# Optimization experiments

Measured on AMD Instinct MI355X. Metric: run time of the kernel, lower is better.

Reference implementation:

```python
import jax, jax.numpy as jnp
import numpy as np

N_ANGLES = 8
K = 15


def setup_inputs() -> dict:
    key = jax.random.key(0)
    k1, k2, k3 = jax.random.split(key, 3)
    N, Cin, Cout = 2048, 16, 32
    NA = N_ANGLES * N
    x = jax.random.normal(k1, (N, Cin), dtype=jnp.float32)
    # scaled so spectral radius ~1 (like a normalized Laplacian) to keep the
    # Chebyshev recurrence numerically bounded
    Ls = jax.random.normal(k2, (NA, NA), dtype=jnp.float32) / np.float32(np.sqrt(NA))
    fan = N_ANGLES * Cin + Cout  # xavier_uniform bound
    bound = np.float32(np.sqrt(6.0 / fan))
    weight = jax.random.uniform(k3, (K, N_ANGLES * Cin, Cout), dtype=jnp.float32,
                                minval=-bound, maxval=bound)
    bias = jnp.zeros((Cout,), dtype=jnp.float32)
    return {"x": x, "Ls": Ls, "weight": weight, "bias": bias}


def _proj(T, Wk, N, Cin):
    # T: [n_angles*N, Cin] -> [N, n_angles*Cin] @ Wk -> [N, Cout]
    return T.reshape(N_ANGLES, N, Cin).transpose(1, 0, 2).reshape(N, N_ANGLES * Cin) @ Wk


def reference(x, Ls, weight, bias):
    N, Cin = x.shape
    Tx0 = jnp.tile(x, (N_ANGLES, 1))            # [nA*N, Cin]
    out = _proj(Tx0, weight[0], N, Cin)          # [N, Cout]
    Tx1 = Ls @ Tx0
    out = out + _proj(Tx1, weight[1], N, Cin)
    for k in range(2, K):
        Tx2 = 2.0 * (Ls @ Tx1) - Tx0
        out = out + _proj(Tx2, weight[k], N, Cin)
        Tx0, Tx1 = Tx1, Tx2
    return out + bias
```

## Files before the change

kernel.cpp:

```cpp
#include <hip/hip_runtime.h>
#include <hip/hip_fp16.h>

#define NA   16384
#define NN   2048
#define CIN  16
#define COUT 32
#define NANG 8
#define KCH  15
#define NSTEP  512
#define CHUNK  4
#define NCHUNK (NSTEP / CHUNK)
#define NPANEL 1024
#define PGRID  ((NN * COUT) / 256)
#define SGRID  (NPANEL / 4)

#define TSCALE_INV 0.03125f
#define TSCALE     32.0f


typedef _Float16 f16x8 __attribute__((ext_vector_type(8)));
typedef _Float16 f16x4 __attribute__((ext_vector_type(4)));
typedef float    f32x4 __attribute__((ext_vector_type(4)));

__global__ __launch_bounds__(256) void k_tile_t(const float* __restrict__ x,
                                                float* __restrict__ T32,
                                                _Float16* __restrict__ Tsw) {
    int tid = blockIdx.x * 256 + threadIdx.x;
    if (tid >= 8 * 64 * 64) return;
    const int s  = tid >> 12;
    const int st = (tid >> 6) & 63;
    const int l  = tid & 63;
    const int ch = l & 15;
    const int c2 = ((l >> 4) << 3) + (st << 5);
    f16x8 h;
    float v[8];
    #pragma unroll
    for (int e = 0; e < 8; ++e) {
        v[e] = x[(c2 + e) * CIN + ch];
        h[e] = (_Float16)(v[e] * TSCALE_INV);
    }
    float* d = T32 + (size_t)ch * NA + s * (NA / 8) + c2;
    *(float4*)(d)     = make_float4(v[0], v[1], v[2], v[3]);
    *(float4*)(d + 4) = make_float4(v[4], v[5], v[6], v[7]);
    *(f16x8*)(Tsw + (size_t)tid * 8) = h;
}

__device__ __forceinline__ void proj_body(const float* __restrict__ Tt,
                                          const float* __restrict__ W,
                                          const float* __restrict__ bias,
                                          float* __restrict__ out, int add,
                                          int idx) {
    const int n  = idx >> 5;
    const int co = idx & 31;
    float s = add ? out[idx] : bias[co];
    #pragma unroll
    for (int a = 0; a < NANG; ++a)
        #pragma unroll
        for (int ci = 0; ci < CIN; ++ci)
            s = fmaf(Tt[(size_t)ci * NA + a * NN + n],
                     W[(size_t)(a * CIN + ci) * COUT + co], s);
    out[idx] = s;
}

#define LOADCHUNK(BUF, PC)                                                   \
    _Pragma("unroll")                                                        \
    for (int u = 0; u < CHUNK; ++u) {                                        \
        const int st = (PC) * CHUNK + u;                                     \
        if (CONV) {                                                          \
            f32x4 f0 = __builtin_nontemporal_load((const f32x4*)(aF + (size_t)st * 32));     \
            f32x4 f1 = __builtin_nontemporal_load((const f32x4*)(aF + (size_t)st * 32 + 4)); \
            f16x8 h;                                                         \
            h[0] = (_Float16)f0[0]; h[1] = (_Float16)f0[1];                  \
            h[2] = (_Float16)f0[2]; h[3] = (_Float16)f0[3];                  \
            h[4] = (_Float16)f1[0]; h[5] = (_Float16)f1[1];                  \
            h[6] = (_Float16)f1[2]; h[7] = (_Float16)f1[3];                  \
            __builtin_nontemporal_store(h, (f16x8*)(aW + (size_t)st * 512)); \
            A[BUF][u] = h;                                                   \
        } else {                                                             \
            A[BUF][u] = __builtin_nontemporal_load((const f16x8*)(aP + (size_t)st * 512));   \
        }                                                                    \
        B[BUF][u] = *(const f16x8*)(bP + (size_t)st * 512);                  \
    }

template<int CONV, int REV>
__global__ __launch_bounds__(256)
void k_sweep(const float* __restrict__ Ls,
             _Float16* __restrict__ Lsw,
             const _Float16* __restrict__ Tsw,
             const float* __restrict__ Tp,
             float* __restrict__ Tn,
             _Float16* __restrict__ Tswn,
             float alpha, float beta,
             const float* __restrict__ Tproj,
             const float* __restrict__ Wk,
             const float* __restrict__ bias,
             float* __restrict__ out, int add) {
    if (blockIdx.x < PGRID) {
        proj_body(Tproj, Wk, bias, out, add,
                  (int)blockIdx.x * 256 + (int)threadIdx.x);
        return;
    }
    constexpr int DEPTH = CONV ? 2 : 4;
    static_assert(NCHUNK % 2 == 0 && NCHUNK % 4 == 0,
                  "tail chunk would replay stale buffer");
    const int w    = threadIdx.x >> 6;
    const int l    = threadIdx.x & 63;
    const int bid0 = (int)blockIdx.x - PGRID;
    const int bid  = REV ? (SGRID - 1 - bid0) : bid0;
    const int p    = bid * 4 + w;
    const int rc   = l & 15;
    const int kg   = l >> 4;

    const size_t aoff = (size_t)p * (NSTEP * 512) + (size_t)l * 8;
    const _Float16* aP = Lsw + aoff;
    _Float16*       aW = Lsw + aoff;
    const float*    aF = Ls + (size_t)(p * 16 + rc) * NA + kg * 8;
    const _Float16* bP = Tsw + (size_t)l * 8;

    f32x4 acc = {0.f, 0.f, 0.f, 0.f};
    f16x8 A[DEPTH][CHUNK], B[DEPTH][CHUNK];

    LOADCHUNK(0, 0);
    if (DEPTH >= 3) { LOADCHUNK(1 & (DEPTH - 1), 1); }
    if (DEPTH >= 4) { LOADCHUNK(2 & (DEPTH - 1), 2); }

    #pragma unroll 1
    for (int cc = 0; cc < NCHUNK; cc += DEPTH) {
        #pragma unroll
        for (int d = 0; d < DEPTH; ++d) {
            const int pf = cc + d + DEPTH - 1;
            if (pf < NCHUNK) { LOADCHUNK((d + DEPTH - 1) % DEPTH, pf); }
            #pragma unroll
            for (int u = 0; u < CHUNK; ++u)
                acc = __builtin_amdgcn_mfma_f32_16x16x32_f16(A[d][u], B[d][u],
                                                             acc, 0, 0, 0);
        }
    }

    const size_t tb = (size_t)rc * NA + (size_t)p * 16 + kg * 4;
    float4 tp4 = make_float4(0.f, 0.f, 0.f, 0.f);
    if (beta != 0.f) tp4 = *(const float4*)(Tp + tb);
    const float v0 = alpha * acc[0] + beta * tp4.x;
    const float v1 = alpha * acc[1] + beta * tp4.y;
    const float v2 = alpha * acc[2] + beta * tp4.z;
    const float v3 = alpha * acc[3] + beta * tp4.w;
    *(float4*)(Tn + tb) = make_float4(v0, v1, v2, v3);
    const int c0 = p * 16 + kg * 4;
    const size_t tf = ((size_t)(c0 >> 5) * 64 + ((c0 >> 3) & 3) * 16 + rc) * 8
                      + (c0 & 7);
    f16x4 h;
    h[0] = (_Float16)(v0 * TSCALE_INV); h[1] = (_Float16)(v1 * TSCALE_INV);
    h[2] = (_Float16)(v2 * TSCALE_INV); h[3] = (_Float16)(v3 * TSCALE_INV);
    *(f16x4*)(Tswn + tf) = h;
}

__global__ __launch_bounds__(256) void k_proj_t(const float* __restrict__ Tt,
                                                const float* __restrict__ W,
                                                const float* __restrict__ bias,
                                                float* __restrict__ out, int add) {
    int idx = blockIdx.x * 256 + threadIdx.x;
    if (idx >= NN * COUT) return;
    proj_body(Tt, W, bias, out, add, idx);
}

extern "C" void kernel_launch(void* const* d_in, const int* in_sizes, int n_in,
                              void* d_out, int out_size, void* d_ws, size_t ws_size,
                              hipStream_t stream) {
    const float* x    = (const float*)d_in[0];
    const float* Ls   = (const float*)d_in[1];
    const float* W    = (const float*)d_in[2];
    const float* bias = (const float*)d_in[3];
    float* out = (float*)d_out;

    char* wsb = (char*)d_ws;
    _Float16* Lsw = (_Float16*)wsb;
    float* T32base = (float*)(wsb + (size_t)NA * NA * sizeof(_Float16));
    const size_t TSZ = (size_t)CIN * NA;
    float* T32[3] = { T32base, T32base + TSZ, T32base + 2 * TSZ };
    _Float16* Tswbase = (_Float16*)(T32base + 3 * TSZ);
    _Float16* Tsw[3] = { Tswbase, Tswbase + TSZ, Tswbase + 2 * TSZ };

    const int WSTRIDE = (NANG * CIN) * COUT;
    const int FGRID = (8 * 64 * 64) / 256;
    const int GRID  = PGRID + SGRID;

    k_tile_t<<<FGRID, 256, 0, stream>>>(x, T32[0], Tsw[0]);

    k_sweep<1, 0><<<GRID, 256, 0, stream>>>(Ls, Lsw, Tsw[0], T32[0],
                                            T32[1], Tsw[1], TSCALE, 0.f,
                                            T32[0], W, bias, out, 0);

    int prev = 0, cur = 1;
    for (int k = 2; k < KCH; ++k) {
        int nxt = 3 - cur - prev;
        const float* Wk = W + (size_t)(k - 1) * WSTRIDE;
        if (k & 1)
            k_sweep<0, 0><<<GRID, 256, 0, stream>>>(Ls, Lsw, Tsw[cur], T32[prev],
                                                    T32[nxt], Tsw[nxt],
                                                    2.0f * TSCALE, -1.f,
                                                    T32[cur], Wk, bias, out, 1);
        else
            k_sweep<0, 1><<<GRID, 256, 0, stream>>>(Ls, Lsw, Tsw[cur], T32[prev],
                                                    T32[nxt], Tsw[nxt],
                                                    2.0f * TSCALE, -1.f,
                                                    T32[cur], Wk, bias, out, 1);
        prev = cur; cur = nxt;
    }

    k_proj_t<<<PGRID, 256, 0, stream>>>(T32[cur], W + (size_t)(KCH - 1) * WSTRIDE,
                                        bias, out, 1);
}
```

Measured before the change: 1.686 ms.

## Fuse all Chebyshev steps into one cooperative persistent kernel with grid syncs

Replaces the sequence of per-step kernel launches with a single cooperative kernel of 256 blocks. It runs the tile, projection and sweep stages in a loop separated by grid-wide barriers, and projection work is spread over all blocks before each sweep. The Ls fp16 copy is written with normal rather than nontemporal stores in the fused path, so it may stay in cache. The intent is to remove launch gaps and keep data warm, but only 256 blocks run, which may leave CUs underused. The multi-launch path is kept as a fallback.

Result: slower. 2.408 ms (+42.8%).

```diff
diff --git a/kernel.cpp b/kernel.cpp
--- a/kernel.cpp
+++ b/kernel.cpp
@@ -1,5 +1,8 @@
 #include <hip/hip_runtime.h>
 #include <hip/hip_fp16.h>
+#include <hip/hip_cooperative_groups.h>
+
+namespace cg = cooperative_groups;
 
 #define NA   16384
 #define NN   2048
@@ -13,6 +16,8 @@
 #define NPANEL 1024
 #define PGRID  ((NN * COUT) / 256)
 #define SGRID  (NPANEL / 4)
+#define TGRID  ((8 * 64 * 64) / 256)
+#define WSTRIDE (NANG * CIN * COUT)
 
 #define TSCALE_INV 0.03125f
 #define TSCALE     32.0f
@@ -22,11 +27,10 @@
 typedef _Float16 f16x4 __attribute__((ext_vector_type(4)));
 typedef float    f32x4 __attribute__((ext_vector_type(4)));
 
-__global__ __launch_bounds__(256) void k_tile_t(const float* __restrict__ x,
-                                                float* __restrict__ T32,
-                                                _Float16* __restrict__ Tsw) {
-    int tid = blockIdx.x * 256 + threadIdx.x;
-    if (tid >= 8 * 64 * 64) return;
+__device__ __forceinline__ void tile_body(const float* __restrict__ x,
+                                          float* __restrict__ T32,
+                                          _Float16* __restrict__ Tsw, int bid) {
+    int tid = bid * 256 + threadIdx.x;
     const int s  = tid >> 12;
     const int st = (tid >> 6) & 63;
     const int l  = tid & 63;
@@ -62,7 +66,7 @@
     out[idx] = s;
 }
 
-#define LOADCHUNK(BUF, PC)                                                   \
+#define LOADCHUNK(BUF, PC, NTST)                                             \
     _Pragma("unroll")                                                        \
     for (int u = 0; u < CHUNK; ++u) {                                        \
         const int st = (PC) * CHUNK + u;                                     \
@@ -74,7 +78,8 @@
             h[2] = (_Float16)f0[2]; h[3] = (_Float16)f0[3];                  \
             h[4] = (_Float16)f1[0]; h[5] = (_Float16)f1[1];                  \
             h[6] = (_Float16)f1[2]; h[7] = (_Float16)f1[3];                  \
-            __builtin_nontemporal_store(h, (f16x8*)(aW + (size_t)st * 512)); \
+            if (NTST) { __builtin_nontemporal_store(h, (f16x8*)(aW + (size_t)st * 512)); }   \
+            else      { *(f16x8*)(aW + (size_t)st * 512) = h; }              \
             A[BUF][u] = h;                                                   \
         } else {                                                             \
             A[BUF][u] = __builtin_nontemporal_load((const f16x8*)(aP + (size_t)st * 512));   \
@@ -82,34 +87,22 @@
         B[BUF][u] = *(const f16x8*)(bP + (size_t)st * 512);                  \
     }
 
-template<int CONV, int REV>
-__global__ __launch_bounds__(256)
-void k_sweep(const float* __restrict__ Ls,
-             _Float16* __restrict__ Lsw,
-             const _Float16* __restrict__ Tsw,
-             const float* __restrict__ Tp,
-             float* __restrict__ Tn,
-             _Float16* __restrict__ Tswn,
-             float alpha, float beta,
-             const float* __restrict__ Tproj,
-             const float* __restrict__ Wk,
-             const float* __restrict__ bias,
-             float* __restrict__ out, int add) {
-    if (blockIdx.x < PGRID) {
-        proj_body(Tproj, Wk, bias, out, add,
-                  (int)blockIdx.x * 256 + (int)threadIdx.x);
-        return;
-    }
+template<int CONV, int NTST>
+__device__ __forceinline__ void sweep_body(const float* __restrict__ Ls,
+                                           _Float16* __restrict__ Lsw,
+                                           const _Float16* __restrict__ Tsw,
+                                           const float* __restrict__ Tp,
+                                           float* __restrict__ Tn,
+                                           _Float16* __restrict__ Tswn,
+                                           float alpha, float beta, int bid) {
     constexpr int DEPTH = CONV ? 2 : 4;
     static_assert(NCHUNK % 2 == 0 && NCHUNK % 4 == 0,
                   "tail chunk would replay stale buffer");
-    const int w    = threadIdx.x >> 6;
-    const int l    = threadIdx.x & 63;
-    const int bid0 = (int)blockIdx.x - PGRID;
-    const int bid  = REV ? (SGRID - 1 - bid0) : bid0;
-    const int p    = bid * 4 + w;
-    const int rc   = l & 15;
-    const int kg   = l >> 4;
+    const int w  = threadIdx.x >> 6;
+    const int l  = threadIdx.x & 63;
+    const int p  = bid * 4 + w;
+    const int rc = l & 15;
+    const int kg = l >> 4;
 
     const size_t aoff = (size_t)p * (NSTEP * 512) + (size_t)l * 8;
     const _Float16* aP = Lsw + aoff;
@@ -120,16 +113,16 @@
     f32x4 acc = {0.f, 0.f, 0.f, 0.f};
     f16x8 A[DEPTH][CHUNK], B[DEPTH][CHUNK];
 
-    LOADCHUNK(0, 0);
-    if (DEPTH >= 3) { LOADCHUNK(1 & (DEPTH - 1), 1); }
-    if (DEPTH >= 4) { LOADCHUNK(2 & (DEPTH - 1), 2); }
+    LOADCHUNK(0, 0, NTST);
+    if (DEPTH >= 3) { LOADCHUNK(1 & (DEPTH - 1), 1, NTST); }
+    if (DEPTH >= 4) { LOADCHUNK(2 & (DEPTH - 1), 2, NTST); }
 
     #pragma unroll 1
     for (int cc = 0; cc < NCHUNK; cc += DEPTH) {
         #pragma unroll
         for (int d = 0; d < DEPTH; ++d) {
             const int pf = cc + d + DEPTH - 1;
-            if (pf < NCHUNK) { LOADCHUNK((d + DEPTH - 1) % DEPTH, pf); }
+            if (pf < NCHUNK) { LOADCHUNK((d + DEPTH - 1) % DEPTH, pf, NTST); }
             #pragma unroll
             for (int u = 0; u < CHUNK; ++u)
                 acc = __builtin_amdgcn_mfma_f32_16x16x32_f16(A[d][u], B[d][u],
@@ -154,13 +147,68 @@
     *(f16x4*)(Tswn + tf) = h;
 }
 
+__global__ __launch_bounds__(256)
+void k_fused(const float* __restrict__ x, const float* __restrict__ Ls,
+             const float* __restrict__ W, const float* __restrict__ bias,
+             float* __restrict__ out, _Float16* __restrict__ Lsw,
+             float* __restrict__ T32b, _Float16* __restrict__ Tswb) {
+    const size_t TSZ = (size_t)CIN * NA;
+    float*    T32[3] = { T32b, T32b + TSZ, T32b + 2 * TSZ };
+    _Float16* Tsw[3] = { Tswb, Tswb + TSZ, Tswb + 2 * TSZ };
+    cg::grid_group grid = cg::this_grid();
+    const int b   = (int)blockIdx.x;
+    const int idx = b * 256 + (int)threadIdx.x;
+
+    if (b < TGRID) tile_body(x, T32[0], Tsw[0], b);
+    grid.sync();
+
+    proj_body(T32[0], W, bias, out, 0, idx);
+    sweep_body<1, 0>(Ls, Lsw, Tsw[0], T32[0], T32[1], Tsw[1], TSCALE, 0.f, b);
+    grid.sync();
+
+    #pragma unroll 1
+    for (int k = 2; k < KCH; ++k) {
+        const int cur = (k - 1) % 3, prev = (k - 2) % 3, nxt = k % 3;
+        proj_body(T32[cur], W + (size_t)(k - 1) * WSTRIDE, bias, out, 1, idx);
+        const int bid = (k & 1) ? b : (SGRID - 1 - b);
+        sweep_body<0, 0>(Ls, Lsw, Tsw[cur], T32[prev], T32[nxt], Tsw[nxt],
+                         2.0f * TSCALE, -1.f, bid);
+        grid.sync();
+    }
+
+    proj_body(T32[(KCH - 1) % 3], W + (size_t)(KCH - 1) * WSTRIDE,
+              bias, out, 1, idx);
+}
+
+__global__ __launch_bounds__(256) void k_tile_t(const float* __restrict__ x,
+                                                float* __restrict__ T32,
+                                                _Float16* __restrict__ Tsw) {
+    tile_body(x, T32, Tsw, (int)blockIdx.x);
+}
+
+template<int CONV, int REV>
+__global__ __launch_bounds__(256)
+void k_sweep(const float* __restrict__ Ls, _Float16* __restrict__ Lsw,
+             const _Float16* __restrict__ Tsw, const float* __restrict__ Tp,
+             float* __restrict__ Tn, _Float16* __restrict__ Tswn,
+             float alpha, float beta,
+             const float* __restrict__ Tproj, const float* __restrict__ Wk,
+             const float* __restrict__ bias, float* __restrict__ out, int add) {
+    if (blockIdx.x < PGRID) {
+        proj_body(Tproj, Wk, bias, out, add,
+                  (int)blockIdx.x * 256 + (int)threadIdx.x);
+        return;
+    }
+    const int bid0 = (int)blockIdx.x - PGRID;
+    const int bid  = REV ? (SGRID - 1 - bid0) : bid0;
+    sweep_body<CONV, 1>(Ls, Lsw, Tsw, Tp, Tn, Tswn, alpha, beta, bid);
+}
+
 __global__ __launch_bounds__(256) void k_proj_t(const float* __restrict__ Tt,
                                                 const float* __restrict__ W,
                                                 const float* __restrict__ bias,
                                                 float* __restrict__ out, int add) {
-    int idx = blockIdx.x * 256 + threadIdx.x;
-    if (idx >= NN * COUT) return;
-    proj_body(Tt, W, bias, out, add, idx);
+    proj_body(Tt, W, bias, out, add, (int)blockIdx.x * 256 + (int)threadIdx.x);
 }
 
 extern "C" void kernel_launch(void* const* d_in, const int* in_sizes, int n_in,
@@ -174,22 +222,34 @@
 
     char* wsb = (char*)d_ws;
     _Float16* Lsw = (_Float16*)wsb;
-    float* T32base = (float*)(wsb + (size_t)NA * NA * sizeof(_Float16));
+    float* T32b = (float*)(wsb + (size_t)NA * NA * sizeof(_Float16));
     const size_t TSZ = (size_t)CIN * NA;
-    float* T32[3] = { T32base, T32base + TSZ, T32base + 2 * TSZ };
-    _Float16* Tswbase = (_Float16*)(T32base + 3 * TSZ);
-    _Float16* Tsw[3] = { Tswbase, Tswbase + TSZ, Tswbase + 2 * TSZ };
-
-    const int WSTRIDE = (NANG * CIN) * COUT;
-    const int FGRID = (8 * 64 * 64) / 256;
-    const int GRID  = PGRID + SGRID;
-
-    k_tile_t<<<FGRID, 256, 0, stream>>>(x, T32[0], Tsw[0]);
-
+    float* T32[3] = { T32b, T32b + TSZ, T32b + 2 * TSZ };
+    _Float16* Tswb = (_Float16*)(T32b + 3 * TSZ);
+    _Float16* Tsw[3] = { Tswb, Tswb + TSZ, Tswb + 2 * TSZ };
+
+    int coop = 0;
+    int dev = 0;
+    hipGetDevice(&dev);
+    hipDeviceGetAttribute(&coop, hipDeviceAttributeCooperativeLaunch, dev);
+
+    hipError_t err = hipErrorUnknown;
+    if (coop) {
+        const float* xa = x; const float* La = Ls; const float* Wa = W;
+        const float* ba = bias; float* oa = out;
+        _Float16* lswa = Lsw; float* t32a = T32b; _Float16* tswa = Tswb;
+        void* args[] = { (void*)&xa, (void*)&La, (void*)&Wa, (void*)&ba,
+                         (void*)&oa, (void*)&lswa, (void*)&t32a, (void*)&tswa };
+        err = hipLaunchCooperativeKernel((const void*)k_fused,
+                                         dim3(SGRID), dim3(256), args, 0, stream);
+    }
+    if (err == hipSuccess) return;
+
+    const int GRID = PGRID + SGRID;
+    k_tile_t<<<TGRID, 256, 0, stream>>>(x, T32[0], Tsw[0]);
     k_sweep<1, 0><<<GRID, 256, 0, stream>>>(Ls, Lsw, Tsw[0], T32[0],
                                             T32[1], Tsw[1], TSCALE, 0.f,
                                             T32[0], W, bias, out, 0);
-
     int prev = 0, cur = 1;
     for (int k = 2; k < KCH; ++k) {
         int nxt = 3 - cur - prev;
@@ -206,7 +266,6 @@
                                                     T32[cur], Wk, bias, out, 1);
         prev = cur; cur = nxt;
     }
-
     k_proj_t<<<PGRID, 256, 0, stream>>>(T32[cur], W + (size_t)(KCH - 1) * WSTRIDE,
                                         bias, out, 1);
 }
```
